# Kernel optimization log

Hardware: AMD Instinct MI355X
Metric: run time of the kernel (lower is better)

Reference implementation:

```python
import jax, jax.numpy as jnp
import numpy as np
import math

B, S, D, H = 4, 1024, 1024, 16
HD = D // H  # head_size = 64
NEG = -1e9


def setup_inputs() -> dict:
    rng = jax.random.key(0)
    ks = jax.random.split(rng, 12)
    f = lambda k, shape: jax.random.normal(k, shape, dtype=jnp.float32)
    inp = {
        "query": f(ks[0], (B, S, D)),
        "key": f(ks[1], (B, S, D)),
        "value": f(ks[2], (B, S, D)),
        # rel: correlation matrix between interactions, non-negative
        "rel": jax.random.uniform(ks[3], (B, S, S), dtype=jnp.float32),
        "l1": jnp.float32(0.5),
        "l2": jnp.float32(0.5),
        # timestamp: |t_i - t_j| time gaps
        "timestamp": jax.random.uniform(ks[4], (B, S, S), dtype=jnp.float32) * 10.0,
        "encode_pos": 0,
        "pos_key_embeds": f(ks[5], (32, HD)) * 0.02,
        "pos_value_embeds": f(ks[6], (32, HD)) * 0.02,
        # causal mask: True = disallowed (future) position
        "mask": jnp.broadcast_to(jnp.triu(jnp.ones((S, S), dtype=bool), k=1), (B, S, S)),
        "Wq": f(ks[7], (D, D)) / math.sqrt(D), "bq": jnp.zeros((D,), jnp.float32),
        "Wk": f(ks[8], (D, D)) / math.sqrt(D), "bk": jnp.zeros((D,), jnp.float32),
        "Wv": f(ks[9], (D, D)) / math.sqrt(D), "bv": jnp.zeros((D,), jnp.float32),
    }
    return inp


def _split_heads(x, W, b):
    # nn.Linear uses x @ W.T + b ; reshape to [B,H,S,HD]
    y = x @ W.T + b
    return y.reshape(B, S, H, HD).transpose(0, 2, 1, 3)


def reference(query, key, value, rel, l1, l2, timestamp, encode_pos,
              pos_key_embeds, pos_value_embeds, mask,
              Wq, bq, Wk, bk, Wv, bv):
    assert encode_pos == 0, "reference implements the encode_pos=False path"
    q = _split_heads(query, Wq, bq)   # [B,H,S,HD]
    k = _split_heads(key, Wk, bk)
    v = _split_heads(value, Wv, bv)

    m = mask[:, None]  # [B,1,S,S], True = masked

    # relation-based attention: future-mask rel, softmax over nonzero entries
    relm = rel[:, None] * (~m).astype(jnp.float32)          # [B,1,S,S]
    rel_attn = jax.nn.softmax(jnp.where(relm == 0, -1e5, relm), axis=-1)

    # scaled dot-product scores
    scores = jnp.einsum("bhqd,bhkd->bhqk", q, k) / jnp.sqrt(jnp.float32(HD))
    scores = jnp.where(m, NEG, scores)
    prob_attn = jax.nn.softmax(scores, axis=-1)             # [B,H,S,S]

    # time-decay attention: exp(-|dt|), future-masked
    ts = jnp.exp(-jnp.abs(timestamp))[:, None]              # [B,1,S,S]
    ts = jnp.where(m, NEG, ts)
    time_attn = jax.nn.softmax(ts, axis=-1)

    prob = (1.0 - l2) * prob_attn + l2 * time_attn
    prob = (1.0 - l1) * prob + l1 * rel_attn                # [B,H,S,S]

    out = jnp.einsum("bhqk,bhkd->bhqd", prob, v)
    out = out.transpose(0, 2, 1, 3).reshape(B, S, D)
    return out, prob
```

## Files before the change

kernel.cpp:

```cpp
#include <hip/hip_runtime.h>
#include <cstdint>
#include <cstddef>


typedef __bf16 bf16_t;
typedef __bf16 bf16x8 __attribute__((ext_vector_type(8)));
typedef __bf16 bf16x4 __attribute__((ext_vector_type(4)));
typedef float  f32x4  __attribute__((ext_vector_type(4)));

__device__ __forceinline__ f32x4 mfma16(bf16x8 a, bf16x8 b, f32x4 c) {
  return __builtin_amdgcn_mfma_f32_16x16x32_bf16(a, b, c, 0, 0, 0);
}

__device__ __forceinline__ void g2l16(const void* g, void* l) {
  __builtin_amdgcn_global_load_lds((__attribute__((address_space(1))) void*)(g),
                                   (__attribute__((address_space(3))) void*)(l),
                                   16, 0, 0);
}

__global__ __launch_bounds__(256) void cast_kernel(
    const float* __restrict__ q, const float* __restrict__ k, const float* __restrict__ v,
    const float* __restrict__ wq, const float* __restrict__ wk, const float* __restrict__ wv,
    bf16_t* __restrict__ Xb, bf16_t* __restrict__ Wb) {
  int i = blockIdx.x * 256 + threadIdx.x;
  const float* src;
  bf16_t* dst;
  if (i < 3145728) {
    int m = i >> 20;
    size_t o = (size_t)(i & 1048575) * 4;
    src = (m == 0) ? q : (m == 1) ? k : v;
    dst = Xb + (size_t)m * 4194304 + o;
    src += o;
  } else {
    int j = i - 3145728;
    int m = j >> 18;
    size_t o = (size_t)(j & 262143) * 4;
    src = (m == 0) ? wq : (m == 1) ? wk : wv;
    dst = Wb + (size_t)m * 1048576 + o;
    src += o;
  }
  f32x4 f = *(const f32x4*)src;
  bf16x4 r;
  r[0] = (bf16_t)f[0]; r[1] = (bf16_t)f[1]; r[2] = (bf16_t)f[2]; r[3] = (bf16_t)f[3];
  *(bf16x4*)dst = r;
}

__global__ __launch_bounds__(256) void gemm_qkv(
    const bf16_t* __restrict__ Xb, const bf16_t* __restrict__ Wb,
    const float* __restrict__ bqp, const float* __restrict__ bkp, const float* __restrict__ bvp,
    bf16_t* __restrict__ Yb) {
  __shared__ __align__(16) bf16_t As[128 * 32];
  __shared__ __align__(16) bf16_t Bs[128 * 32];
  const int z = blockIdx.z;
  const bf16_t* X = Xb + (size_t)z * 4194304;
  const bf16_t* W = Wb + (size_t)z * 1048576;
  const float* bias = (z == 0) ? bqp : (z == 1) ? bkp : bvp;
  bf16_t* Y = Yb + (size_t)z * 4194304;

  const int tid = threadIdx.x;
  const int lane = tid & 63;
  const int w = tid >> 6;
  const int wr = w >> 1, wc = w & 1;
  const int rb = blockIdx.y * 128, cb = blockIdx.x * 128;
  const int lr = lane & 15, g = lane >> 4;

  f32x4 zero = {0.f, 0.f, 0.f, 0.f};
  f32x4 acc[4][4];
  for (int m = 0; m < 4; ++m)
    for (int n = 0; n < 4; ++n) acc[m][n] = zero;

  for (int k0 = 0; k0 < 1024; k0 += 32) {
    for (int r = 0; r < 2; ++r) {
      int cid = r * 256 + tid;
      int row = cid >> 2;
      int ko = (cid & 3) * 8;
      const bf16_t* ga = X + ((size_t)(rb + row) * 1024 + k0 + ko);
      const bf16_t* gb = W + ((size_t)(cb + row) * 1024 + k0 + ko);
      char* la = (char*)As + r * 4096 + w * 1024;
      char* lb = (char*)Bs + r * 4096 + w * 1024;
      g2l16(ga, la);
      g2l16(gb, lb);
    }
    asm volatile("s_waitcnt vmcnt(0)" ::: "memory");
    __syncthreads();

    bf16x8 afr[4], bfr[4];
    for (int m = 0; m < 4; ++m)
      afr[m] = *(const bf16x8*)&As[(wr * 64 + m * 16 + lr) * 32 + g * 8];
    for (int n = 0; n < 4; ++n)
      bfr[n] = *(const bf16x8*)&Bs[(wc * 64 + n * 16 + lr) * 32 + g * 8];
    for (int m = 0; m < 4; ++m)
      for (int n = 0; n < 4; ++n)
        acc[m][n] = mfma16(afr[m], bfr[n], acc[m][n]);
    __syncthreads();
  }

  for (int m = 0; m < 4; ++m) {
    int rowb = rb + wr * 64 + m * 16 + g * 4;
    for (int n = 0; n < 4; ++n) {
      int col = cb + wc * 64 + n * 16 + lr;
      float bb = bias[col];
      for (int r = 0; r < 4; ++r)
        Y[(size_t)(rowb + r) * 1024 + col] = (bf16_t)(acc[m][n][r] + bb);
    }
  }
}

__global__ __launch_bounds__(256) void transpose_v(const bf16_t* __restrict__ Yv,
                                                   bf16_t* __restrict__ vT) {
  __shared__ __align__(16) bf16_t t[64][68];
  const int bh = blockIdx.y, b = bh >> 4, h = bh & 15;
  const int s0 = blockIdx.x * 64;
  const int tid = threadIdx.x;
  for (int i = 0; i < 4; ++i) {
    int c = tid + i * 256;
    int r = c >> 4, c4 = (c & 15) * 4;
    bf16x4 v4 = *(const bf16x4*)(Yv + ((size_t)(b * 1024 + s0 + r)) * 1024 + h * 64 + c4);
    *(bf16x4*)&t[r][c4] = v4;
  }
  __syncthreads();
  for (int i = 0; i < 4; ++i) {
    int c = tid + i * 256;
    int hd = c >> 4, s4 = (c & 15) * 4;
    bf16x4 o;
    o[0] = t[s4 + 0][hd]; o[1] = t[s4 + 1][hd];
    o[2] = t[s4 + 2][hd]; o[3] = t[s4 + 3][hd];
    *(bf16x4*)(vT + ((size_t)(bh * 64 + hd)) * 1024 + s0 + s4) = o;
  }
}

__global__ __launch_bounds__(256) void base_kernel(
    const float* __restrict__ rel, const float* __restrict__ ts,
    const float* __restrict__ l1p, const float* __restrict__ l2p,
    bf16_t* __restrict__ baseb) {
  const int row = blockIdx.x;
  const int q = row & 1023;
  const int tid = threadIdx.x;
  const int w = tid >> 6;
  const float l1 = *l1p, l2 = *l2p;
  const float cr = l1, ct = (1.f - l1) * l2;

  f32x4 rv = *(const f32x4*)(rel + (size_t)row * 1024 + tid * 4);
  f32x4 tv = *(const f32x4*)(ts  + (size_t)row * 1024 + tid * 4);

  float x[4], t[4];
  for (int j = 0; j < 4; ++j) {
    int k = tid * 4 + j;
    bool msk = k > q;
    float rj = rv[j];
    x[j] = (msk || rj == 0.f) ? -100000.f : rj;
    t[j] = msk ? -1e9f : __expf(-fabsf(tv[j]));
  }
  float mr = fmaxf(fmaxf(x[0], x[1]), fmaxf(x[2], x[3]));
  float mt = fmaxf(fmaxf(t[0], t[1]), fmaxf(t[2], t[3]));
  for (int o = 1; o < 64; o <<= 1) {
    mr = fmaxf(mr, __shfl_xor(mr, o));
    mt = fmaxf(mt, __shfl_xor(mt, o));
  }
  __shared__ float red[4][4];
  if ((tid & 63) == 0) { red[0][w] = mr; red[1][w] = mt; }
  __syncthreads();
  mr = fmaxf(fmaxf(red[0][0], red[0][1]), fmaxf(red[0][2], red[0][3]));
  mt = fmaxf(fmaxf(red[1][0], red[1][1]), fmaxf(red[1][2], red[1][3]));

  float er[4], et[4], sr = 0.f, st = 0.f;
  for (int j = 0; j < 4; ++j) {
    er[j] = __expf(x[j] - mr);
    et[j] = __expf(t[j] - mt);
    sr += er[j]; st += et[j];
  }
  for (int o = 1; o < 64; o <<= 1) {
    sr += __shfl_xor(sr, o);
    st += __shfl_xor(st, o);
  }
  if ((tid & 63) == 0) { red[2][w] = sr; red[3][w] = st; }
  __syncthreads();
  sr = red[2][0] + red[2][1] + red[2][2] + red[2][3];
  st = red[3][0] + red[3][1] + red[3][2] + red[3][3];

  float isr = cr / sr, ist = ct / st;
  bf16x4 o4;
  for (int j = 0; j < 4; ++j) o4[j] = (bf16_t)(er[j] * isr + et[j] * ist);
  *(bf16x4*)(baseb + (size_t)row * 1024 + tid * 4) = o4;
}

__global__ __launch_bounds__(256) void attn_kernel(
    const bf16_t* __restrict__ qY, const bf16_t* __restrict__ kY,
    const bf16_t* __restrict__ vT, const bf16_t* __restrict__ baseb,
    const float* __restrict__ l1p, const float* __restrict__ l2p,
    float* __restrict__ outp, float* __restrict__ probp) {
  const int bh = blockIdx.x, b = bh >> 4, h = bh & 15;
  const int qg = 63 - blockIdx.y;
  const int q0 = qg * 16;
  const int tid = threadIdx.x, lane = tid & 63, w = tid >> 6;
  const int lr = lane & 15, g = lane >> 4;
  const int qr = q0 + lr;
  const float l1 = *l1p, l2 = *l2p;
  const float c1 = (1.f - l1) * (1.f - l2);

  __shared__ __align__(16) union ShMem {
    bf16_t plds[4][16][36];
    float  pvred[4][16][64];
  } sh;
  __shared__ float zred[4][16];

  const bf16_t* qbase = qY + ((size_t)(b * 1024 + q0 + lr)) * 1024 + h * 64 + g * 8;
  bf16x8 bq0 = *(const bf16x8*)qbase;
  bf16x8 bq1 = *(const bf16x8*)(qbase + 32);

  const bf16_t* kptr = kY + ((size_t)(b * 1024 + lr)) * 1024 + h * 64 + g * 8;

  const int nch = q0 / 32 + 1;
  f32x4 zero = {0.f, 0.f, 0.f, 0.f};

  bf16x4 esave[8][2];
  float zp = 0.f;
#pragma unroll
  for (int c = 0; c < 8; ++c) {
    const int ch = w + 4 * c;
    if (ch < nch) {
      const bf16_t* p0 = kptr + (size_t)ch * 32768;
      bf16x8 k0 = *(const bf16x8*)p0;
      bf16x8 k1 = *(const bf16x8*)(p0 + 32);
      bf16x8 k2 = *(const bf16x8*)(p0 + 16384);
      bf16x8 k3 = *(const bf16x8*)(p0 + 16416);
      f32x4 s0 = zero, s1 = zero;
      s0 = mfma16(k0, bq0, s0);
      s0 = mfma16(k1, bq1, s0);
      s1 = mfma16(k2, bq0, s1);
      s1 = mfma16(k3, bq1, s1);
      const int kc0 = ch * 32 + g * 4;
      bf16x4 e0, e1;
      for (int r = 0; r < 4; ++r) {
        float ea = (kc0 + r > qr) ? 0.f : __expf(s0[r] * 0.125f);
        float eb = (kc0 + 16 + r > qr) ? 0.f : __expf(s1[r] * 0.125f);
        zp += ea + eb;
        e0[r] = (bf16_t)ea;
        e1[r] = (bf16_t)eb;
      }
      esave[c][0] = e0;
      esave[c][1] = e1;
    }
  }
  zp += __shfl_xor(zp, 16);
  zp += __shfl_xor(zp, 32);
  if (lane < 16) zred[w][lr] = zp;
  __syncthreads();
  const float Z = zred[0][lr] + zred[1][lr] + zred[2][lr] + zred[3][lr];
  const float invz = c1 / Z;

  const bf16_t* baserow = baseb + ((size_t)(b * 1024 + qr)) * 1024;
  const bf16_t* vbase = vT + ((size_t)(bh * 64 + lr)) * 1024 + g * 8;
  float* probbase = probp + ((size_t)(bh * 1024 + q0)) * 1024;
  const int srow = lane >> 3, scol = (lane & 7) * 4;

  f32x4 acc[4];
  for (int cf = 0; cf < 4; ++cf) acc[cf] = zero;

#pragma unroll
  for (int c = 0; c < 8; ++c) {
    const int ch = w + 4 * c;
    if (ch < nch) {
      bf16x8 vv[4];
      for (int cf = 0; cf < 4; ++cf)
        vv[cf] = *(const bf16x8*)(vbase + (size_t)cf * 16384 + ch * 32);
      for (int f = 0; f < 2; ++f) {
        const int kc0 = ch * 32 + f * 16 + g * 4;
        bf16x4 b4 = *(const bf16x4*)(baserow + kc0);
        bf16x4 eb = esave[c][f];
        bf16x4 pb;
        for (int r = 0; r < 4; ++r)
          pb[r] = (bf16_t)((float)eb[r] * invz + (float)b4[r]);
        *(bf16x4*)&sh.plds[w][lr][f * 16 + g * 4] = pb;
      }
      asm volatile("s_waitcnt lgkmcnt(0)" ::: "memory");
      bf16x8 pa = *(const bf16x8*)&sh.plds[w][lr][g * 8];
      bf16x4 r0 = *(const bf16x4*)&sh.plds[w][srow][scol];
      bf16x4 r1 = *(const bf16x4*)&sh.plds[w][srow + 8][scol];
      f32x4 o0, o1;
      for (int j = 0; j < 4; ++j) { o0[j] = (float)r0[j]; o1[j] = (float)r1[j]; }
      float* pr = probbase + (size_t)srow * 1024 + ch * 32 + scol;
      __builtin_nontemporal_store(o0, (f32x4*)pr);
      __builtin_nontemporal_store(o1, (f32x4*)(pr + 8 * 1024));
      for (int cf = 0; cf < 4; ++cf)
        acc[cf] = mfma16(pa, vv[cf], acc[cf]);
    }
  }

  const int kstart = nch * 32;
  for (int i = 0; i < 4; ++i) {
    int qrr = q0 + w * 4 + i;
    const bf16_t* brow = baseb + ((size_t)(b * 1024 + qrr)) * 1024;
    float* prow = probp + ((size_t)(bh * 1024 + qrr)) * 1024;
    for (int k = kstart + lane * 4; k < 1024; k += 256) {
      bf16x4 b4 = *(const bf16x4*)(brow + k);
      f32x4 f4;
      f4[0] = (float)b4[0]; f4[1] = (float)b4[1];
      f4[2] = (float)b4[2]; f4[3] = (float)b4[3];
      __builtin_nontemporal_store(f4, (f32x4*)(prow + k));
    }
  }

  __syncthreads();
  for (int cf = 0; cf < 4; ++cf)
    for (int r = 0; r < 4; ++r)
      sh.pvred[w][g * 4 + r][cf * 16 + lr] = acc[cf][r];
  __syncthreads();
  {
    const int row0 = tid >> 6, hd = tid & 63;
    for (int i = 0; i < 4; ++i) {
      int row = row0 + 4 * i;
      float s = sh.pvred[0][row][hd] + sh.pvred[1][row][hd] +
                sh.pvred[2][row][hd] + sh.pvred[3][row][hd];
      outp[((size_t)(b * 1024 + q0 + row)) * 1024 + h * 64 + hd] = s;
    }
  }
}

extern "C" void kernel_launch(void* const* d_in, const int* in_sizes, int n_in,
                              void* d_out, int out_size, void* d_ws, size_t ws_size,
                              hipStream_t stream) {
  const float* query = (const float*)d_in[0];
  const float* key   = (const float*)d_in[1];
  const float* value = (const float*)d_in[2];
  const float* rel   = (const float*)d_in[3];
  const float* l1p   = (const float*)d_in[4];
  const float* l2p   = (const float*)d_in[5];
  const float* tsp   = (const float*)d_in[6];
  const float* Wq = (const float*)d_in[11];
  const float* bq = (const float*)d_in[12];
  const float* Wk = (const float*)d_in[13];
  const float* bk = (const float*)d_in[14];
  const float* Wv = (const float*)d_in[15];
  const float* bv = (const float*)d_in[16];

  char* ws = (char*)d_ws;
  bf16_t* Xb    = (bf16_t*)(ws);
  bf16_t* Wb    = (bf16_t*)(ws + 25165824);
  bf16_t* Yb    = (bf16_t*)(ws + 31457280);
  bf16_t* vT    = (bf16_t*)(ws + 56623104);
  bf16_t* baseb = (bf16_t*)(ws + 65011712);

  float* outp  = (float*)d_out;
  float* probp = outp + 4194304;

  cast_kernel<<<dim3(15360), dim3(256), 0, stream>>>(query, key, value, Wq, Wk, Wv, Xb, Wb);
  gemm_qkv<<<dim3(8, 32, 3), dim3(256), 0, stream>>>(Xb, Wb, bq, bk, bv, Yb);
  transpose_v<<<dim3(16, 64), dim3(256), 0, stream>>>(Yb + (size_t)2 * 4194304, vT);
  base_kernel<<<dim3(4096), dim3(256), 0, stream>>>(rel, tsp, l1p, l2p, baseb);
  attn_kernel<<<dim3(64, 64), dim3(256), 0, stream>>>(Yb, Yb + 4194304, vT, baseb,
                                                      l1p, l2p, outp, probp);
}
```

Before: 172.4 us.

## Process two 16-row query tiles per 512-thread block with swizzled block order

The attention kernel now uses 512 threads per block, with two groups of four waves each handling a separate 16-row query tile. The grid becomes a 1D launch of 2048 blocks. Block ids are remapped so that consecutive blocks spread across batch-head pairs while the causal-heavy query tiles are scheduled first. The intent is to halve the block count, share launch and scheduling overhead, and improve load balance and L2 locality. In exchange each block needs more LDS and registers, which may reduce occupancy.

```diff
diff --git a/kernel.cpp b/kernel.cpp
--- a/kernel.cpp
+++ b/kernel.cpp
@@ -184,40 +184,45 @@
   *(bf16x4*)(baseb + (size_t)row * 1024 + tid * 4) = o4;
 }
 
-__global__ __launch_bounds__(256) void attn_kernel(
+__global__ __launch_bounds__(512) void attn_kernel(
     const bf16_t* __restrict__ qY, const bf16_t* __restrict__ kY,
     const bf16_t* __restrict__ vT, const bf16_t* __restrict__ baseb,
     const float* __restrict__ l1p, const float* __restrict__ l2p,
     float* __restrict__ outp, float* __restrict__ probp) {
-  const int bh = blockIdx.x, b = bh >> 4, h = bh & 15;
-  const int qg = 63 - blockIdx.y;
-  const int q0 = qg * 16;
+  const int bid = blockIdx.x;
+  const int j = bid >> 3;
+  const int bh = (bid & 7) * 8 + (j & 7);
+  const int qg = 31 - (j >> 3);
+  const int b = bh >> 4, h = bh & 15;
+  const int q0 = qg * 32;
   const int tid = threadIdx.x, lane = tid & 63, w = tid >> 6;
+  const int t = w >> 2;
+  const int cw = w & 3;
   const int lr = lane & 15, g = lane >> 4;
-  const int qr = q0 + lr;
+  const int qr = q0 + t * 16 + lr;
   const float l1 = *l1p, l2 = *l2p;
   const float c1 = (1.f - l1) * (1.f - l2);
 
   __shared__ __align__(16) union ShMem {
-    bf16_t plds[4][16][36];
-    float  pvred[4][16][64];
+    bf16_t plds[8][16][36];
+    float  pvred[8][16][64];
   } sh;
-  __shared__ float zred[4][16];
-
-  const bf16_t* qbase = qY + ((size_t)(b * 1024 + q0 + lr)) * 1024 + h * 64 + g * 8;
+  __shared__ float zred[8][16];
+
+  const bf16_t* qbase = qY + ((size_t)(b * 1024 + qr)) * 1024 + h * 64 + g * 8;
   bf16x8 bq0 = *(const bf16x8*)qbase;
   bf16x8 bq1 = *(const bf16x8*)(qbase + 32);
 
   const bf16_t* kptr = kY + ((size_t)(b * 1024 + lr)) * 1024 + h * 64 + g * 8;
 
-  const int nch = q0 / 32 + 1;
+  const int nch = (q0 + t * 16) / 32 + 1;
   f32x4 zero = {0.f, 0.f, 0.f, 0.f};
 
   bf16x4 esave[8][2];
   float zp = 0.f;
 #pragma unroll
   for (int c = 0; c < 8; ++c) {
-    const int ch = w + 4 * c;
+    const int ch = cw + 4 * c;
     if (ch < nch) {
       const bf16_t* p0 = kptr + (size_t)ch * 32768;
       bf16x8 k0 = *(const bf16x8*)p0;
@@ -246,12 +251,13 @@
   zp += __shfl_xor(zp, 32);
   if (lane < 16) zred[w][lr] = zp;
   __syncthreads();
-  const float Z = zred[0][lr] + zred[1][lr] + zred[2][lr] + zred[3][lr];
+  const float Z = zred[t * 4 + 0][lr] + zred[t * 4 + 1][lr] +
+                  zred[t * 4 + 2][lr] + zred[t * 4 + 3][lr];
   const float invz = c1 / Z;
 
   const bf16_t* baserow = baseb + ((size_t)(b * 1024 + qr)) * 1024;
   const bf16_t* vbase = vT + ((size_t)(bh * 64 + lr)) * 1024 + g * 8;
-  float* probbase = probp + ((size_t)(bh * 1024 + q0)) * 1024;
+  float* probbase = probp + ((size_t)(bh * 1024 + q0 + t * 16)) * 1024;
   const int srow = lane >> 3, scol = (lane & 7) * 4;
 
   f32x4 acc[4];
@@ -259,7 +265,7 @@
 
 #pragma unroll
   for (int c = 0; c < 8; ++c) {
-    const int ch = w + 4 * c;
+    const int ch = cw + 4 * c;
     if (ch < nch) {
       bf16x8 vv[4];
       for (int cf = 0; cf < 4; ++cf)
@@ -278,7 +284,7 @@
       bf16x4 r0 = *(const bf16x4*)&sh.plds[w][srow][scol];
       bf16x4 r1 = *(const bf16x4*)&sh.plds[w][srow + 8][scol];
       f32x4 o0, o1;
-      for (int j = 0; j < 4; ++j) { o0[j] = (float)r0[j]; o1[j] = (float)r1[j]; }
+      for (int jj = 0; jj < 4; ++jj) { o0[jj] = (float)r0[jj]; o1[jj] = (float)r1[jj]; }
       float* pr = probbase + (size_t)srow * 1024 + ch * 32 + scol;
       __builtin_nontemporal_store(o0, (f32x4*)pr);
       __builtin_nontemporal_store(o1, (f32x4*)(pr + 8 * 1024));
@@ -289,7 +295,7 @@
 
   const int kstart = nch * 32;
   for (int i = 0; i < 4; ++i) {
-    int qrr = q0 + w * 4 + i;
+    int qrr = q0 + t * 16 + cw * 4 + i;
     const bf16_t* brow = baseb + ((size_t)(b * 1024 + qrr)) * 1024;
     float* prow = probp + ((size_t)(bh * 1024 + qrr)) * 1024;
     for (int k = kstart + lane * 4; k < 1024; k += 256) {
@@ -307,12 +313,13 @@
       sh.pvred[w][g * 4 + r][cf * 16 + lr] = acc[cf][r];
   __syncthreads();
   {
-    const int row0 = tid >> 6, hd = tid & 63;
+    const int gw = tid >> 6, hd = tid & 63;
+    const int tt = gw >> 2;
     for (int i = 0; i < 4; ++i) {
-      int row = row0 + 4 * i;
-      float s = sh.pvred[0][row][hd] + sh.pvred[1][row][hd] +
-                sh.pvred[2][row][hd] + sh.pvred[3][row][hd];
-      outp[((size_t)(b * 1024 + q0 + row)) * 1024 + h * 64 + hd] = s;
+      int rr = (gw & 3) * 4 + i;
+      float s = sh.pvred[tt * 4 + 0][rr][hd] + sh.pvred[tt * 4 + 1][rr][hd] +
+                sh.pvred[tt * 4 + 2][rr][hd] + sh.pvred[tt * 4 + 3][rr][hd];
+      outp[((size_t)(b * 1024 + q0 + tt * 16 + rr)) * 1024 + h * 64 + hd] = s;
     }
   }
 }
@@ -348,6 +355,6 @@
   gemm_qkv<<<dim3(8, 32, 3), dim3(256), 0, stream>>>(Xb, Wb, bq, bk, bv, Yb);
   transpose_v<<<dim3(16, 64), dim3(256), 0, stream>>>(Yb + (size_t)2 * 4194304, vT);
   base_kernel<<<dim3(4096), dim3(256), 0, stream>>>(rel, tsp, l1p, l2p, baseb);
-  attn_kernel<<<dim3(64, 64), dim3(256), 0, stream>>>(Yb, Yb + 4194304, vT, baseb,
-                                                      l1p, l2p, outp, probp);
-}
+  attn_kernel<<<dim3(2048), dim3(512), 0, stream>>>(Yb, Yb + 4194304, vT, baseb,
+                                                    l1p, l2p, outp, probp);
+}
```

Result: no change. 171.9 us (-0.3%).
